# Optimization experiments

Measured on AMD Instinct MI355X. Metric: run time of the kernel, lower is better.

The kernel has to match this reference:

```python
import jax, jax.numpy as jnp
import numpy as np

N, C, H = 4096, 768, 12
HD = C // H
SCALE = HD ** -0.5


def setup_inputs() -> dict:
    key = jax.random.key(0)
    k1, k2, k3 = jax.random.split(key, 3)
    x = jax.random.normal(k1, (N, C), dtype=jnp.float32)
    w_qkv = jax.random.normal(k2, (C, 3 * C), dtype=jnp.float32) * (C ** -0.5)
    w_proj = jax.random.normal(k3, (C, C), dtype=jnp.float32) * (C ** -0.5)
    b_proj = jnp.zeros((C,), dtype=jnp.float32)
    return {"x": x, "w_qkv": w_qkv, "w_proj": w_proj, "b_proj": b_proj}


def reference(x, w_qkv, w_proj, b_proj):
    n, c = x.shape
    # fused QKV projection (qkv_bias=False): [N, 3C] -> [3, H, N, hd]
    qkv = (x @ w_qkv).reshape(n, 3, H, HD)
    qkv = jnp.transpose(qkv, (1, 2, 0, 3))  # (3, H, N, hd)
    q, k, v = qkv[0], qkv[1], qkv[2]
    # scaled dot-product attention per head: (H, N, N)
    attn = jnp.einsum('hnd,hmd->hnm', q, k) * SCALE
    attn = jax.nn.softmax(attn, axis=-1)
    # attn_drop is identity (rate=0, eval mode)
    out = jnp.einsum('hnm,hmd->hnd', attn, v)          # (H, N, hd)
    out = jnp.transpose(out, (1, 0, 2)).reshape(n, c)  # (N, C)
    # output projection (bias by default in nn.Dense); proj_drop identity
    return out @ w_proj + b_proj
```

## Files before the change

### kernel.cpp

```cpp
#include <hip/hip_runtime.h>

#define N_TOK 4096
#define C_DIM 768
#define H_NUM 12
#define QKV_N 2304

typedef __attribute__((ext_vector_type(8))) short bf16x8;
typedef __attribute__((ext_vector_type(4))) float f32x4;
typedef __attribute__((ext_vector_type(16))) float f32x16;
typedef __attribute__((ext_vector_type(4))) unsigned int u32x4;

static __device__ __forceinline__ unsigned short f2bf(float f) {
  unsigned u = __builtin_bit_cast(unsigned, f);
  u += 0x7FFF + ((u >> 16) & 1);
  return (unsigned short)(u >> 16);
}

static __device__ __forceinline__ float bf2f(unsigned short u) {
  return __builtin_bit_cast(float, (unsigned)u << 16);
}

static __device__ __forceinline__ float exp2_fast(float x) {
  float r; asm("v_exp_f32 %0, %1" : "=v"(r) : "v"(x)); return r;
}

#define GLOAD_LDS16(g, l)                                                     \
  __builtin_amdgcn_global_load_lds(                                           \
      (const __attribute__((address_space(1))) void*)(g),                     \
      (__attribute__((address_space(3))) void*)(l), 16, 0, 0)

#define Q_SCALE 0.18033688011112042f

__global__ __launch_bounds__(256) void prep_fused(
    const float* __restrict__ wq, unsigned short* __restrict__ wqT,
    const float* __restrict__ x, unsigned short* __restrict__ xb) {
  __shared__ unsigned short T[64][65];
  const int t = threadIdx.x;
  if (blockIdx.x < 432) {
    const int tid = blockIdx.x;
    const int n0 = (tid % 36) * 64, k0 = (tid / 36) * 64;
    {
      const int r = t >> 2, qd = t & 3;
#pragma unroll
      for (int i = 0; i < 4; ++i) {
        const int c = qd * 16 + i * 4;
        const float4 v = *reinterpret_cast<const float4*>(
            &wq[(size_t)(k0 + r) * QKV_N + n0 + c]);
        T[r][c + 0] = f2bf(v.x); T[r][c + 1] = f2bf(v.y);
        T[r][c + 2] = f2bf(v.z); T[r][c + 3] = f2bf(v.w);
      }
    }
    __syncthreads();
#pragma unroll
    for (int i = 0; i < 2; ++i) {
      const int cid = t + i * 256;
      const int rn = cid >> 3, cx = cid & 7;
      unsigned short tmp[8];
#pragma unroll
      for (int j = 0; j < 8; ++j) tmp[j] = T[cx * 8 + j][rn];
      *reinterpret_cast<bf16x8*>(&wqT[(size_t)(n0 + rn) * 768 + k0 + cx * 8]) =
          *reinterpret_cast<bf16x8*>(tmp);
    }
  } else {
    const int i = (blockIdx.x - 432) * 256 + t;
    const float4 a = reinterpret_cast<const float4*>(x)[i * 2];
    const float4 b = reinterpret_cast<const float4*>(x)[i * 2 + 1];
    unsigned short tmp[8] = {f2bf(a.x), f2bf(a.y), f2bf(a.z), f2bf(a.w),
                             f2bf(b.x), f2bf(b.y), f2bf(b.z), f2bf(b.w)};
    reinterpret_cast<bf16x8*>(xb)[i] = *reinterpret_cast<bf16x8*>(tmp);
  }
}

__global__ __launch_bounds__(256) void transpose_cvt(
    const float* __restrict__ in, unsigned short* __restrict__ out,
    int K, int N) {
  __shared__ unsigned short T[64][65];
  const int t = threadIdx.x;
  const int k0 = blockIdx.y * 64, n0 = blockIdx.x * 64;
  {
    const int r = t >> 2, qd = t & 3;
#pragma unroll
    for (int i = 0; i < 4; ++i) {
      const int c = qd * 16 + i * 4;
      const float4 v = *reinterpret_cast<const float4*>(
          &in[(size_t)(k0 + r) * N + n0 + c]);
      T[r][c + 0] = f2bf(v.x); T[r][c + 1] = f2bf(v.y);
      T[r][c + 2] = f2bf(v.z); T[r][c + 3] = f2bf(v.w);
    }
  }
  __syncthreads();
#pragma unroll
  for (int i = 0; i < 2; ++i) {
    const int cid = t + i * 256;
    const int rn = cid >> 3, cx = cid & 7;
    unsigned short tmp[8];
#pragma unroll
    for (int j = 0; j < 8; ++j) tmp[j] = T[cx * 8 + j][rn];
    *reinterpret_cast<bf16x8*>(&out[(size_t)(n0 + rn) * K + k0 + cx * 8]) =
        *reinterpret_cast<bf16x8*>(tmp);
  }
}

__global__ __launch_bounds__(256) void gemm_qkv_bf16(
    const unsigned short* __restrict__ A, const unsigned short* __restrict__ Bt,
    unsigned short* __restrict__ qw, unsigned short* __restrict__ kw,
    unsigned short* __restrict__ vw) {
  __shared__ unsigned short As[128 * 32];
  __shared__ unsigned short Bs[128 * 32];
  const int t = threadIdx.x;
  const int lane = t & 63, wid = t >> 6;
  const int lr = lane & 15, lg = lane >> 4;
  const int lid = blockIdx.y * 18 + blockIdx.x;
  const int swz = (lid & 7) * 72 + (lid >> 3);
  const int m_base = (swz / 18) * 128, n_base = (swz % 18) * 128;
  const int wm = (wid >> 1) * 64, wn = (wid & 1) * 64;
  const int c_row = lane >> 2;
  const int c_col = (lane & 3) * 8;

  f32x4 acc[4][4];
#pragma unroll
  for (int mt = 0; mt < 4; ++mt)
#pragma unroll
    for (int nt = 0; nt < 4; ++nt) acc[mt][nt] = (f32x4){0.f, 0.f, 0.f, 0.f};

  for (int kt = 0; kt < 24; ++kt) {
    const int k0 = kt * 32;
    __syncthreads();
#pragma unroll
    for (int i = 0; i < 2; ++i) {
      const int ch = wid * 2 + i;
      GLOAD_LDS16(&A[(size_t)(m_base + ch * 16 + c_row) * 768 + k0 + c_col],
                  &As[ch * 512]);
      GLOAD_LDS16(&Bt[(size_t)(n_base + ch * 16 + c_row) * 768 + k0 + c_col],
                  &Bs[ch * 512]);
    }
    __syncthreads();
    bf16x8 af[4], bfr[4];
#pragma unroll
    for (int mt = 0; mt < 4; ++mt)
      af[mt] = *reinterpret_cast<const bf16x8*>(&As[(wm + mt * 16 + lr) * 32 + lg * 8]);
#pragma unroll
    for (int nt = 0; nt < 4; ++nt)
      bfr[nt] = *reinterpret_cast<const bf16x8*>(&Bs[(wn + nt * 16 + lr) * 32 + lg * 8]);
#pragma unroll
    for (int mt = 0; mt < 4; ++mt)
#pragma unroll
      for (int nt = 0; nt < 4; ++nt)
        acc[mt][nt] = __builtin_amdgcn_mfma_f32_16x16x32_bf16(af[mt], bfr[nt],
                                                              acc[mt][nt], 0, 0, 0);
  }
#pragma unroll
  for (int mt = 0; mt < 4; ++mt)
#pragma unroll
    for (int nt = 0; nt < 4; ++nt)
#pragma unroll
      for (int r = 0; r < 4; ++r) {
        const int m = m_base + wm + mt * 16 + lg * 4 + r;
        const int c = n_base + wn + nt * 16 + lr;
        const float v = acc[mt][nt][r];
        const int which = c / 768;
        const int cc = c - which * 768;
        const int h = cc >> 6, d = cc & 63;
        if (which == 0) {
          qw[((size_t)h * N_TOK + m) * 64 + d] = f2bf(v * Q_SCALE);
        } else if (which == 1) {
          kw[((size_t)h * N_TOK + m) * 64 + d] = f2bf(v);
        } else {
          vw[((size_t)h * 64 + d) * N_TOK + m] = f2bf(v);
        }
      }
}

__global__ __launch_bounds__(256) void gemm_proj_bf16(
    const unsigned short* __restrict__ A, const unsigned short* __restrict__ Bt,
    const float* __restrict__ bias, float* __restrict__ out) {
  __shared__ unsigned short As[128 * 32];
  __shared__ unsigned short Bs[128 * 32];
  const int t = threadIdx.x;
  const int lane = t & 63, wid = t >> 6;
  const int lr = lane & 15, lg = lane >> 4;
  const int lid = blockIdx.y * 6 + blockIdx.x;
  const int swz = (lid & 7) * 24 + (lid >> 3);
  const int m_base = (swz / 6) * 128, n_base = (swz % 6) * 128;
  const int wm = (wid >> 1) * 64, wn = (wid & 1) * 64;
  const int c_row = lane >> 2;
  const int c_col = (lane & 3) * 8;

  f32x4 acc[4][4];
#pragma unroll
  for (int mt = 0; mt < 4; ++mt)
#pragma unroll
    for (int nt = 0; nt < 4; ++nt) acc[mt][nt] = (f32x4){0.f, 0.f, 0.f, 0.f};

  for (int kt = 0; kt < 24; ++kt) {
    const int k0 = kt * 32;
    __syncthreads();
#pragma unroll
    for (int i = 0; i < 2; ++i) {
      const int ch = wid * 2 + i;
      GLOAD_LDS16(&A[(size_t)(m_base + ch * 16 + c_row) * 768 + k0 + c_col],
                  &As[ch * 512]);
      GLOAD_LDS16(&Bt[(size_t)(n_base + ch * 16 + c_row) * 768 + k0 + c_col],
                  &Bs[ch * 512]);
    }
    __syncthreads();
    bf16x8 af[4], bfr[4];
#pragma unroll
    for (int mt = 0; mt < 4; ++mt)
      af[mt] = *reinterpret_cast<const bf16x8*>(&As[(wm + mt * 16 + lr) * 32 + lg * 8]);
#pragma unroll
    for (int nt = 0; nt < 4; ++nt)
      bfr[nt] = *reinterpret_cast<const bf16x8*>(&Bs[(wn + nt * 16 + lr) * 32 + lg * 8]);
#pragma unroll
    for (int mt = 0; mt < 4; ++mt)
#pragma unroll
      for (int nt = 0; nt < 4; ++nt)
        acc[mt][nt] = __builtin_amdgcn_mfma_f32_16x16x32_bf16(af[mt], bfr[nt],
                                                              acc[mt][nt], 0, 0, 0);
  }
#pragma unroll
  for (int nt = 0; nt < 4; ++nt) {
    const int n = n_base + wn + nt * 16 + lr;
    const float bv = bias[n];
#pragma unroll
    for (int mt = 0; mt < 4; ++mt)
#pragma unroll
      for (int r = 0; r < 4; ++r) {
        const int m = m_base + wm + mt * 16 + lg * 4 + r;
        out[(size_t)m * 768 + n] = acc[mt][nt][r] + bv;
      }
  }
}

__global__ __launch_bounds__(256) void attn_kernel(
    const unsigned short* __restrict__ qw, const unsigned short* __restrict__ kw,
    const unsigned short* __restrict__ vw, unsigned short* __restrict__ po0,
    unsigned short* __restrict__ po1, float* __restrict__ lw) {
  __shared__ unsigned short smem[9216];
  const int t = threadIdx.x;
  const int lane = t & 63;
  const int qsub = t >> 6;
  const int q31 = lane & 31;
  const int hi = lane >> 5;
  const int swz = (blockIdx.x & 7) * 96 + (blockIdx.x >> 3);
  const int h = swz >> 6;
  const int rem = swz & 63;
  const int half = rem >> 5;
  const int qst = rem & 31;
  const int q0 = qst * 128 + qsub * 32;

  unsigned short* Ks = smem;
  unsigned short* Vs = smem + 4608;

  const unsigned short* kbase = &kw[(size_t)h * N_TOK * 64];
  const unsigned short* vbase = &vw[(size_t)h * 64 * N_TOK];
  const int kv0 = half * 2048;

  bf16x8 qf[4];
#pragma unroll
  for (int ks = 0; ks < 4; ++ks)
    qf[ks] = *reinterpret_cast<const bf16x8*>(
        &qw[((size_t)h * N_TOK + q0 + q31) * 64 + ks * 16 + hi * 8]);

  f32x16 acc0, acc1;
#pragma unroll
  for (int r = 0; r < 16; ++r) { acc0[r] = 0.f; acc1[r] = 0.f; }
  float l_run = 0.f;

  const int srow0 = t >> 3;
  const int srow1 = (t + 256) >> 3;
  const int sseg = (t & 7) * 8;

  bf16x8 kst[2], vst[2];
  {
    kst[0] = *reinterpret_cast<const bf16x8*>(&kbase[(size_t)(kv0 + srow0) * 64 + sseg]);
    kst[1] = *reinterpret_cast<const bf16x8*>(&kbase[(size_t)(kv0 + srow1) * 64 + sseg]);
    vst[0] = *reinterpret_cast<const bf16x8*>(&vbase[(size_t)srow0 * N_TOK + kv0 + sseg]);
    vst[1] = *reinterpret_cast<const bf16x8*>(&vbase[(size_t)srow1 * N_TOK + kv0 + sseg]);
  }

  for (int kvt = 0; kvt < 32; ++kvt) {
    const int kv = kv0 + kvt * 64;
    __syncthreads();
    *reinterpret_cast<bf16x8*>(&Ks[srow0 * 72 + sseg]) = kst[0];
    *reinterpret_cast<bf16x8*>(&Ks[srow1 * 72 + sseg]) = kst[1];
    *reinterpret_cast<bf16x8*>(&Vs[srow0 * 72 + sseg]) = vst[0];
    *reinterpret_cast<bf16x8*>(&Vs[srow1 * 72 + sseg]) = vst[1];
    __syncthreads();
    const int kvn = (kvt + 1 < 32) ? kv + 64 : kv0;
    kst[0] = *reinterpret_cast<const bf16x8*>(&kbase[(size_t)(kvn + srow0) * 64 + sseg]);
    kst[1] = *reinterpret_cast<const bf16x8*>(&kbase[(size_t)(kvn + srow1) * 64 + sseg]);
    vst[0] = *reinterpret_cast<const bf16x8*>(&vbase[(size_t)srow0 * N_TOK + kvn + sseg]);
    vst[1] = *reinterpret_cast<const bf16x8*>(&vbase[(size_t)srow1 * N_TOK + kvn + sseg]);

#pragma unroll
    for (int ct = 0; ct < 2; ++ct) {
      f32x16 s;
#pragma unroll
      for (int r = 0; r < 16; ++r) s[r] = 0.f;
      __builtin_amdgcn_s_setprio(1);
#pragma unroll
      for (int ks = 0; ks < 4; ++ks) {
        const bf16x8 kf = *reinterpret_cast<const bf16x8*>(
            &Ks[(ct * 32 + q31) * 72 + ks * 16 + hi * 8]);
        s = __builtin_amdgcn_mfma_f32_32x32x16_bf16(kf, qf[ks], s, 0, 0, 0);
      }
      __builtin_amdgcn_s_setprio(0);

      float p[16];
#pragma unroll
      for (int r = 0; r < 16; ++r) p[r] = exp2_fast(s[r]);
      float s8[8];
#pragma unroll
      for (int r = 0; r < 8; ++r) s8[r] = p[r] + p[r + 8];
#pragma unroll
      for (int r = 0; r < 4; ++r) s8[r] = s8[r] + s8[r + 4];
      l_run += (s8[0] + s8[1]) + (s8[2] + s8[3]);

      unsigned dw[8];
#pragma unroll
      for (int m2 = 0; m2 < 8; ++m2)
        asm("v_cvt_pk_bf16_f32 %0, %1, %2"
            : "=v"(dw[m2]) : "v"(p[2 * m2]), "v"(p[2 * m2 + 1]));
      asm("v_permlane32_swap_b32 %0, %1" : "+v"(dw[0]), "+v"(dw[2]));
      asm("v_permlane32_swap_b32 %0, %1" : "+v"(dw[1]), "+v"(dw[3]));
      asm("v_permlane32_swap_b32 %0, %1" : "+v"(dw[4]), "+v"(dw[6]));
      asm("v_permlane32_swap_b32 %0, %1" : "+v"(dw[5]), "+v"(dw[7]));

      __builtin_amdgcn_s_setprio(1);
#pragma unroll
      for (int ksl = 0; ksl < 2; ++ksl) {
        u32x4 u;
        u.x = dw[ksl * 4 + 0]; u.y = dw[ksl * 4 + 1];
        u.z = dw[ksl * 4 + 2]; u.w = dw[ksl * 4 + 3];
        const bf16x8 pa = __builtin_bit_cast(bf16x8, u);
        const int kg = ct * 2 + ksl;
        const bf16x8 vf0 = *reinterpret_cast<const bf16x8*>(
            &Vs[q31 * 72 + kg * 16 + hi * 8]);
        const bf16x8 vf1 = *reinterpret_cast<const bf16x8*>(
            &Vs[(32 + q31) * 72 + kg * 16 + hi * 8]);
        acc0 = __builtin_amdgcn_mfma_f32_32x32x16_bf16(pa, vf0, acc0, 0, 0, 0);
        acc1 = __builtin_amdgcn_mfma_f32_32x32x16_bf16(pa, vf1, acc1, 0, 0, 0);
      }
      __builtin_amdgcn_s_setprio(0);
    }
  }

  l_run += __shfl_xor(l_run, 32);
  const float linv = 1.0f / l_run;
  unsigned short* pout = half ? po1 : po0;
#pragma unroll
  for (int r = 0; r < 16; ++r) {
    const int crow = (r & 3) + 8 * (r >> 2) + 4 * hi;
    const float iv = __shfl(linv, crow);
    const size_t base = (size_t)(q0 + crow) * C_DIM + h * 64;
    pout[base + q31] = f2bf(acc0[r] * iv);
    pout[base + 32 + q31] = f2bf(acc1[r] * iv);
  }
  if (hi == 0) lw[half * 49152 + h * 4096 + q0 + q31] = l_run;
}

__global__ __launch_bounds__(256) void attn_merge(
    unsigned short* __restrict__ po0, const unsigned short* __restrict__ po1,
    const float* __restrict__ lw) {
  const int i = blockIdx.x * 256 + threadIdx.x;
  const int base = i * 8;
  const int q = base / 768;
  const int c = base - q * 768;
  const int h = c >> 6;
  const float l0 = lw[h * 4096 + q];
  const float l1 = lw[49152 + h * 4096 + q];
  const float w = 1.0f / (l0 + l1);
  const float w0 = l0 * w, w1 = l1 * w;
  const bf16x8 a = *reinterpret_cast<const bf16x8*>(&po0[base]);
  const bf16x8 b = *reinterpret_cast<const bf16x8*>(&po1[base]);
  unsigned short tmp[8];
#pragma unroll
  for (int j = 0; j < 8; ++j)
    tmp[j] = f2bf(w0 * bf2f((unsigned short)a[j]) +
                  w1 * bf2f((unsigned short)b[j]));
  *reinterpret_cast<bf16x8*>(&po0[base]) = *reinterpret_cast<bf16x8*>(tmp);
}

extern "C" void kernel_launch(void* const* d_in, const int* in_sizes, int n_in,
                              void* d_out, int out_size, void* d_ws, size_t ws_size,
                              hipStream_t stream) {
  (void)in_sizes; (void)n_in; (void)out_size; (void)ws_size;
  const float* x = (const float*)d_in[0];
  const float* w_qkv = (const float*)d_in[1];
  const float* w_proj = (const float*)d_in[2];
  const float* b_proj = (const float*)d_in[3];
  float* out = (float*)d_out;

  const size_t HNd = (size_t)H_NUM * N_TOK * 64;
  unsigned short* qw = (unsigned short*)d_ws;
  unsigned short* kw = qw + HNd;
  unsigned short* vw = kw + HNd;
  unsigned short* xb = vw + HNd;
  unsigned short* ow = xb;
  unsigned short* wT = xb + HNd;
  unsigned short* wqkvT = wT;
  unsigned short* wprojT = wT;
  unsigned short* po1 = wT + HNd;
  float* lw = (float*)(po1 + HNd);

  prep_fused<<<dim3(1968), 256, 0, stream>>>(w_qkv, wqkvT, x, xb);
  gemm_qkv_bf16<<<dim3(QKV_N / 128, N_TOK / 128), 256, 0, stream>>>(
      xb, wqkvT, qw, kw, vw);
  transpose_cvt<<<dim3(C_DIM / 64, C_DIM / 64), 256, 0, stream>>>(
      w_proj, wprojT, C_DIM, C_DIM);
  attn_kernel<<<dim3(768), 256, 0, stream>>>(qw, kw, vw, ow, po1, lw);
  attn_merge<<<dim3(N_TOK * C_DIM / 8 / 256), 256, 0, stream>>>(ow, po1, lw);
  gemm_proj_bf16<<<dim3(C_DIM / 128, N_TOK / 128), 256, 0, stream>>>(
      ow, wprojT, b_proj, out);
}
```

Before: 139.7 us.

## Double-buffer K/V tiles via direct global-to-LDS loads with XOR swizzle

The attention kernel now stages K and V tiles straight from global memory into LDS with a global-load-to-LDS macro. It uses two LDS buffers, so the next tile's load overlaps compute on the current one, and drops the register staging and the second barrier. The padded 72-element rows become 64-element rows with an XOR chunk swizzle to avoid bank conflicts. LDS use rises from 18 KB to 32 KB per block, which may reduce occupancy. A vmcnt(0) wait at the top of each iteration serialises against the prefetch.

```diff
diff --git a/kernel.cpp b/kernel.cpp
--- a/kernel.cpp
+++ b/kernel.cpp
@@ -236,12 +236,13 @@
     const unsigned short* __restrict__ qw, const unsigned short* __restrict__ kw,
     const unsigned short* __restrict__ vw, unsigned short* __restrict__ po0,
     unsigned short* __restrict__ po1, float* __restrict__ lw) {
-  __shared__ unsigned short smem[9216];
+  __shared__ unsigned short smem[16384];
   const int t = threadIdx.x;
   const int lane = t & 63;
   const int qsub = t >> 6;
   const int q31 = lane & 31;
   const int hi = lane >> 5;
+  const int q7 = q31 & 7;
   const int swz = (blockIdx.x & 7) * 96 + (blockIdx.x >> 3);
   const int h = swz >> 6;
   const int rem = swz & 63;
@@ -249,13 +250,14 @@
   const int qst = rem & 31;
   const int q0 = qst * 128 + qsub * 32;
 
-  unsigned short* Ks = smem;
-  unsigned short* Vs = smem + 4608;
-
   const unsigned short* kbase = &kw[(size_t)h * N_TOK * 64];
   const unsigned short* vbase = &vw[(size_t)h * 64 * N_TOK];
   const int kv0 = half * 2048;
 
+  const int lr8 = lane >> 3;
+  const int lc8 = lane & 7;
+  const int sck = lc8 ^ lr8;
+
   bf16x8 qf[4];
 #pragma unroll
   for (int ks = 0; ks < 4; ++ks)
@@ -267,31 +269,34 @@
   for (int r = 0; r < 16; ++r) { acc0[r] = 0.f; acc1[r] = 0.f; }
   float l_run = 0.f;
 
-  const int srow0 = t >> 3;
-  const int srow1 = (t + 256) >> 3;
-  const int sseg = (t & 7) * 8;
-
-  bf16x8 kst[2], vst[2];
-  {
-    kst[0] = *reinterpret_cast<const bf16x8*>(&kbase[(size_t)(kv0 + srow0) * 64 + sseg]);
-    kst[1] = *reinterpret_cast<const bf16x8*>(&kbase[(size_t)(kv0 + srow1) * 64 + sseg]);
-    vst[0] = *reinterpret_cast<const bf16x8*>(&vbase[(size_t)srow0 * N_TOK + kv0 + sseg]);
-    vst[1] = *reinterpret_cast<const bf16x8*>(&vbase[(size_t)srow1 * N_TOK + kv0 + sseg]);
-  }
-
+#pragma unroll
+  for (int i = 0; i < 2; ++i) {
+    const int rowblk = (qsub * 2 + i) * 8;
+    GLOAD_LDS16(&kbase[(size_t)(kv0 + rowblk + lr8) * 64 + sck * 8],
+                &smem[rowblk * 64]);
+    GLOAD_LDS16(&vbase[(size_t)(rowblk + lr8) * N_TOK + kv0 + sck * 8],
+                &smem[4096 + rowblk * 64]);
+  }
+
+  int cur = 0;
   for (int kvt = 0; kvt < 32; ++kvt) {
-    const int kv = kv0 + kvt * 64;
-    __syncthreads();
-    *reinterpret_cast<bf16x8*>(&Ks[srow0 * 72 + sseg]) = kst[0];
-    *reinterpret_cast<bf16x8*>(&Ks[srow1 * 72 + sseg]) = kst[1];
-    *reinterpret_cast<bf16x8*>(&Vs[srow0 * 72 + sseg]) = vst[0];
-    *reinterpret_cast<bf16x8*>(&Vs[srow1 * 72 + sseg]) = vst[1];
-    __syncthreads();
-    const int kvn = (kvt + 1 < 32) ? kv + 64 : kv0;
-    kst[0] = *reinterpret_cast<const bf16x8*>(&kbase[(size_t)(kvn + srow0) * 64 + sseg]);
-    kst[1] = *reinterpret_cast<const bf16x8*>(&kbase[(size_t)(kvn + srow1) * 64 + sseg]);
-    vst[0] = *reinterpret_cast<const bf16x8*>(&vbase[(size_t)srow0 * N_TOK + kvn + sseg]);
-    vst[1] = *reinterpret_cast<const bf16x8*>(&vbase[(size_t)srow1 * N_TOK + kvn + sseg]);
+    asm volatile("s_waitcnt vmcnt(0)" ::: "memory");
+    __syncthreads();
+    if (kvt + 1 < 32) {
+      const int kvn = kv0 + (kvt + 1) * 64;
+      unsigned short* nb = &smem[(cur ^ 1) * 8192];
+#pragma unroll
+      for (int i = 0; i < 2; ++i) {
+        const int rowblk = (qsub * 2 + i) * 8;
+        GLOAD_LDS16(&kbase[(size_t)(kvn + rowblk + lr8) * 64 + sck * 8],
+                    &nb[rowblk * 64]);
+        GLOAD_LDS16(&vbase[(size_t)(rowblk + lr8) * N_TOK + kvn + sck * 8],
+                    &nb[4096 + rowblk * 64]);
+      }
+    }
+    const unsigned short* Ks = &smem[cur * 8192];
+    const unsigned short* Vs = Ks + 4096;
+    cur ^= 1;
 
 #pragma unroll
     for (int ct = 0; ct < 2; ++ct) {
@@ -302,7 +307,7 @@
 #pragma unroll
       for (int ks = 0; ks < 4; ++ks) {
         const bf16x8 kf = *reinterpret_cast<const bf16x8*>(
-            &Ks[(ct * 32 + q31) * 72 + ks * 16 + hi * 8]);
+            &Ks[(ct * 32 + q31) * 64 + (((ks * 2 + hi) ^ q7) << 3)]);
         s = __builtin_amdgcn_mfma_f32_32x32x16_bf16(kf, qf[ks], s, 0, 0, 0);
       }
       __builtin_amdgcn_s_setprio(0);
@@ -335,10 +340,11 @@
         u.z = dw[ksl * 4 + 2]; u.w = dw[ksl * 4 + 3];
         const bf16x8 pa = __builtin_bit_cast(bf16x8, u);
         const int kg = ct * 2 + ksl;
+        const int vchk = ((kg * 2 + hi) ^ q7) << 3;
         const bf16x8 vf0 = *reinterpret_cast<const bf16x8*>(
-            &Vs[q31 * 72 + kg * 16 + hi * 8]);
+            &Vs[q31 * 64 + vchk]);
         const bf16x8 vf1 = *reinterpret_cast<const bf16x8*>(
-            &Vs[(32 + q31) * 72 + kg * 16 + hi * 8]);
+            &Vs[(32 + q31) * 64 + vchk]);
         acc0 = __builtin_amdgcn_mfma_f32_32x32x16_bf16(pa, vf0, acc0, 0, 0, 0);
         acc1 = __builtin_amdgcn_mfma_f32_32x32x16_bf16(pa, vf1, acc1, 0, 0, 0);
       }
```

After: 139.1 us. No clear change (-0.5%).
